# Kernel tuning notes

Measured on AMD Instinct MI355X. Metric: run time of the kernel, lower is better.

## Reference

```python
import jax, jax.numpy as jnp
import numpy as np

COST_CLASS = 1.0
COST_BBOX = 5.0
COST_GIOU = 2.0


def box_cxcywh_to_xyxy(b):
    cx, cy, w, h = b[..., 0], b[..., 1], b[..., 2], b[..., 3]
    return jnp.stack([cx - 0.5 * w, cy - 0.5 * h, cx + 0.5 * w, cy + 0.5 * h], axis=-1)


def generalized_box_iou(a, b):
    # a: [N,4] xyxy, b: [M,4] xyxy -> [N,M]
    area_a = (a[:, 2] - a[:, 0]) * (a[:, 3] - a[:, 1])
    area_b = (b[:, 2] - b[:, 0]) * (b[:, 3] - b[:, 1])
    lt = jnp.maximum(a[:, None, :2], b[None, :, :2])
    rb = jnp.minimum(a[:, None, 2:], b[None, :, 2:])
    wh = jnp.clip(rb - lt, 0.0)
    inter = wh[..., 0] * wh[..., 1]
    union = area_a[:, None] + area_b[None, :] - inter
    iou = inter / union
    lt_e = jnp.minimum(a[:, None, :2], b[None, :, :2])
    rb_e = jnp.maximum(a[:, None, 2:], b[None, :, 2:])
    wh_e = jnp.clip(rb_e - lt_e, 0.0)
    area_e = wh_e[..., 0] * wh_e[..., 1]
    return iou - (area_e - union) / area_e


def setup_inputs() -> dict:
    key = jax.random.key(0)
    k1, k2, k3, k4 = jax.random.split(key, 4)
    bs, Q, C, T = 64, 300, 13, 32
    pred_logits = jax.random.normal(k1, (bs, Q, C), dtype=jnp.float32)
    pred_boxes = jax.random.uniform(k2, (bs, Q, 4), dtype=jnp.float32)
    tgt_boxes = jax.random.uniform(k3, (bs, T, 4), dtype=jnp.float32)
    tgt_ids = jax.random.randint(k4, (bs, T), 0, 12, dtype=jnp.int64)
    return {"pred_logits": pred_logits, "pred_boxes": pred_boxes,
            "tgt_boxes": tgt_boxes, "tgt_ids": tgt_ids}


def reference(pred_logits, pred_boxes, tgt_boxes, tgt_ids):
    bs, Q, _ = pred_logits.shape
    T = tgt_boxes.shape[1]
    out_prob = jax.nn.softmax(pred_logits.reshape(bs * Q, -1), axis=-1)
    out_bbox = pred_boxes.reshape(bs * Q, 4)
    tgt_bbox = tgt_boxes.reshape(bs * T, 4)
    tgt_id = tgt_ids.reshape(bs * T)
    # classification cost: -P[tgt class]  [bs*Q, bs*T]
    cost_class = -out_prob[:, tgt_id]
    # L1 cdist  [bs*Q, bs*T]
    cost_bbox = jnp.sum(jnp.abs(out_bbox[:, None, :] - tgt_bbox[None, :, :]), axis=-1)
    # -GIoU  [bs*Q, bs*T]
    cost_giou = -generalized_box_iou(box_cxcywh_to_xyxy(out_bbox),
                                     box_cxcywh_to_xyxy(tgt_bbox))
    C = COST_CLASS * cost_class + COST_BBOX * cost_bbox + COST_GIOU * cost_giou
    C = C.reshape(bs, Q, bs * T)
    # faithful to the source: each batch element keeps the FIRST size[i] columns
    # (uniform sizes => [:, :, :T])
    return C[:, :, :T]
```

## Files before the change

kernel.cpp:

```cpp
#include <hip/hip_runtime.h>


constexpr int QN = 300;
constexpr int NC = 13;
constexpr int T  = 32;
constexpr float W_BBOX = 5.0f;
constexpr float W_GIOU = 2.0f;

constexpr int BLK = 256;
constexpr int TPQ = 8;
constexpr int TGT = T / TPQ;

__global__ __launch_bounds__(BLK) void matcher_kernel(
    const float* __restrict__ pred_logits,
    const float* __restrict__ pred_boxes,
    const float* __restrict__ tgt_boxes,
    const int*   __restrict__ tgt_ids,
    float* __restrict__ out)
{
    const int gtid = blockIdx.x * BLK + threadIdx.x;
    const int q   = gtid >> 3;
    const int sub = gtid & 7;

    const float* lg = pred_logits + (size_t)q * NC;
    float l[NC];
    #pragma unroll
    for (int c = 0; c < NC; ++c) l[c] = lg[c];
    float m = l[0];
    #pragma unroll
    for (int c = 1; c < NC; ++c) m = fmaxf(m, l[c]);
    float s = 0.0f;
    #pragma unroll
    for (int c = 0; c < NC; ++c) { l[c] = __expf(l[c] - m); s += l[c]; }
    float inv = 1.0f / s;
    #pragma unroll
    for (int c = 0; c < NC; ++c) l[c] *= inv;

    float4 pb = *(const float4*)(pred_boxes + (size_t)q * 4);
    float px0 = pb.x - 0.5f * pb.z, py0 = pb.y - 0.5f * pb.w;
    float px1 = pb.x + 0.5f * pb.z, py1 = pb.y + 0.5f * pb.w;
    float parea = (px1 - px0) * (py1 - py0);

    const int t0 = sub * TGT;
    float res[TGT];
    #pragma unroll
    for (int k = 0; k < TGT; ++k) {
        const int t = t0 + k;
        float4 tb = *(const float4*)(tgt_boxes + t * 4);
        int id = tgt_ids[t];

        float p = l[0];
        #pragma unroll
        for (int c = 1; c < NC; ++c) p = (id == c) ? l[c] : p;

        float cb = fabsf(pb.x - tb.x) + fabsf(pb.y - tb.y)
                 + fabsf(pb.z - tb.z) + fabsf(pb.w - tb.w);

        float tx0 = tb.x - 0.5f * tb.z, ty0 = tb.y - 0.5f * tb.w;
        float tx1 = tb.x + 0.5f * tb.z, ty1 = tb.y + 0.5f * tb.w;
        float tarea = (tx1 - tx0) * (ty1 - ty0);

        float ltx = fmaxf(px0, tx0), lty = fmaxf(py0, ty0);
        float rbx = fminf(px1, tx1), rby = fminf(py1, ty1);
        float iw = fmaxf(rbx - ltx, 0.0f), ih = fmaxf(rby - lty, 0.0f);
        float inter = iw * ih;
        float uni = parea + tarea - inter;
        float iou = inter / uni;
        float ex0 = fminf(px0, tx0), ey0 = fminf(py0, ty0);
        float ex1 = fmaxf(px1, tx1), ey1 = fmaxf(py1, ty1);
        float earea = (ex1 - ex0) * (ey1 - ey0);
        float giou = iou - (earea - uni) / earea;

        res[k] = -p + W_BBOX * cb - W_GIOU * giou;
    }

    float* o = out + (size_t)q * T + t0;
    float4 v; v.x = res[0]; v.y = res[1]; v.z = res[2]; v.w = res[3];
    *(float4*)o = v;
}

extern "C" void kernel_launch(void* const* d_in, const int* in_sizes, int n_in,
                              void* d_out, int out_size, void* d_ws, size_t ws_size,
                              hipStream_t stream) {
    const float* pred_logits = (const float*)d_in[0];
    const float* pred_boxes  = (const float*)d_in[1];
    const float* tgt_boxes   = (const float*)d_in[2];
    const int*   tgt_ids     = (const int*)d_in[3];
    float* out = (float*)d_out;

    const int total = 64 * QN * TPQ;
    const int grid = total / BLK;
    matcher_kernel<<<grid, BLK, 0, stream>>>(pred_logits, pred_boxes,
                                             tgt_boxes, tgt_ids, out);
}
```

Before: 9.910 us.

## Split softmax across 16 lanes per query with shuffles and lane gather

Each query is now handled by 16 lanes instead of 8. Each lane loads one logit, and the max and sum reductions run cooperatively through xor shuffles, replacing the redundant per-thread 13-element softmax. The class probability for each target is fetched by a lane shuffle indexed by the target id rather than a 13-way select chain. Each lane now computes 2 targets instead of 4, which doubles the thread count and adds shuffle latency, and the stores become float2 instead of float4.

```diff
diff --git a/kernel.cpp b/kernel.cpp
--- a/kernel.cpp
+++ b/kernel.cpp
@@ -8,8 +8,30 @@
 constexpr float W_GIOU = 2.0f;
 
 constexpr int BLK = 256;
-constexpr int TPQ = 8;
-constexpr int TGT = T / TPQ;
+constexpr int LPQ = 16;
+constexpr int QPB = BLK / LPQ;
+
+__device__ __forceinline__ float cost_one(
+    float4 pb, float px0, float py0, float px1, float py1, float parea,
+    float4 tb, float p)
+{
+    float cb = fabsf(pb.x - tb.x) + fabsf(pb.y - tb.y)
+             + fabsf(pb.z - tb.z) + fabsf(pb.w - tb.w);
+    float tx0 = tb.x - 0.5f * tb.z, ty0 = tb.y - 0.5f * tb.w;
+    float tx1 = tb.x + 0.5f * tb.z, ty1 = tb.y + 0.5f * tb.w;
+    float tarea = (tx1 - tx0) * (ty1 - ty0);
+    float ltx = fmaxf(px0, tx0), lty = fmaxf(py0, ty0);
+    float rbx = fminf(px1, tx1), rby = fminf(py1, ty1);
+    float iw = fmaxf(rbx - ltx, 0.0f), ih = fmaxf(rby - lty, 0.0f);
+    float inter = iw * ih;
+    float uni = parea + tarea - inter;
+    float iou = inter / uni;
+    float ex0 = fminf(px0, tx0), ey0 = fminf(py0, ty0);
+    float ex1 = fmaxf(px1, tx1), ey1 = fmaxf(py1, ty1);
+    float earea = (ex1 - ex0) * (ey1 - ey0);
+    float giou = iou - (earea - uni) / earea;
+    return -p + W_BBOX * cb - W_GIOU * giou;
+}
 
 __global__ __launch_bounds__(BLK) void matcher_kernel(
     const float* __restrict__ pred_logits,
@@ -18,65 +40,38 @@
     const int*   __restrict__ tgt_ids,
     float* __restrict__ out)
 {
-    const int gtid = blockIdx.x * BLK + threadIdx.x;
-    const int q   = gtid >> 3;
-    const int sub = gtid & 7;
+    const int tid = threadIdx.x;
+    const int j = tid & (LPQ - 1);
+    const int q = blockIdx.x * QPB + (tid >> 4);
 
-    const float* lg = pred_logits + (size_t)q * NC;
-    float l[NC];
+    float lv = (j < NC) ? pred_logits[(size_t)q * NC + j] : -1e30f;
+    float m = lv;
     #pragma unroll
-    for (int c = 0; c < NC; ++c) l[c] = lg[c];
-    float m = l[0];
+    for (int mask = 8; mask >= 1; mask >>= 1)
+        m = fmaxf(m, __shfl_xor(m, mask, LPQ));
+    float e = (j < NC) ? __expf(lv - m) : 0.0f;
+    float s = e;
     #pragma unroll
-    for (int c = 1; c < NC; ++c) m = fmaxf(m, l[c]);
-    float s = 0.0f;
-    #pragma unroll
-    for (int c = 0; c < NC; ++c) { l[c] = __expf(l[c] - m); s += l[c]; }
-    float inv = 1.0f / s;
-    #pragma unroll
-    for (int c = 0; c < NC; ++c) l[c] *= inv;
+    for (int mask = 8; mask >= 1; mask >>= 1)
+        s += __shfl_xor(s, mask, LPQ);
+    float prob = e / s;
 
     float4 pb = *(const float4*)(pred_boxes + (size_t)q * 4);
     float px0 = pb.x - 0.5f * pb.z, py0 = pb.y - 0.5f * pb.w;
     float px1 = pb.x + 0.5f * pb.z, py1 = pb.y + 0.5f * pb.w;
     float parea = (px1 - px0) * (py1 - py0);
 
-    const int t0 = sub * TGT;
-    float res[TGT];
-    #pragma unroll
-    for (int k = 0; k < TGT; ++k) {
-        const int t = t0 + k;
-        float4 tb = *(const float4*)(tgt_boxes + t * 4);
-        int id = tgt_ids[t];
+    int2 ids = *(const int2*)(tgt_ids + 2 * j);
+    float4 tb0 = *(const float4*)(tgt_boxes + (size_t)(2 * j) * 4);
+    float4 tb1 = *(const float4*)(tgt_boxes + (size_t)(2 * j + 1) * 4);
+    float p0 = __shfl(prob, ids.x, LPQ);
+    float p1 = __shfl(prob, ids.y, LPQ);
 
-        float p = l[0];
-        #pragma unroll
-        for (int c = 1; c < NC; ++c) p = (id == c) ? l[c] : p;
+    float c0 = cost_one(pb, px0, py0, px1, py1, parea, tb0, p0);
+    float c1 = cost_one(pb, px0, py0, px1, py1, parea, tb1, p1);
 
-        float cb = fabsf(pb.x - tb.x) + fabsf(pb.y - tb.y)
-                 + fabsf(pb.z - tb.z) + fabsf(pb.w - tb.w);
-
-        float tx0 = tb.x - 0.5f * tb.z, ty0 = tb.y - 0.5f * tb.w;
-        float tx1 = tb.x + 0.5f * tb.z, ty1 = tb.y + 0.5f * tb.w;
-        float tarea = (tx1 - tx0) * (ty1 - ty0);
-
-        float ltx = fmaxf(px0, tx0), lty = fmaxf(py0, ty0);
-        float rbx = fminf(px1, tx1), rby = fminf(py1, ty1);
-        float iw = fmaxf(rbx - ltx, 0.0f), ih = fmaxf(rby - lty, 0.0f);
-        float inter = iw * ih;
-        float uni = parea + tarea - inter;
-        float iou = inter / uni;
-        float ex0 = fminf(px0, tx0), ey0 = fminf(py0, ty0);
-        float ex1 = fmaxf(px1, tx1), ey1 = fmaxf(py1, ty1);
-        float earea = (ex1 - ex0) * (ey1 - ey0);
-        float giou = iou - (earea - uni) / earea;
-
-        res[k] = -p + W_BBOX * cb - W_GIOU * giou;
-    }
-
-    float* o = out + (size_t)q * T + t0;
-    float4 v; v.x = res[0]; v.y = res[1]; v.z = res[2]; v.w = res[3];
-    *(float4*)o = v;
+    float2 v; v.x = c0; v.y = c1;
+    *(float2*)(out + (size_t)q * T + 2 * j) = v;
 }
 
 extern "C" void kernel_launch(void* const* d_in, const int* in_sizes, int n_in,
@@ -88,8 +83,8 @@
     const int*   tgt_ids     = (const int*)d_in[3];
     float* out = (float*)d_out;
 
-    const int total = 64 * QN * TPQ;
-    const int grid = total / BLK;
+    const int total_q = 64 * QN;
+    const int grid = total_q / QPB;
     matcher_kernel<<<grid, BLK, 0, stream>>>(pred_logits, pred_boxes,
                                              tgt_boxes, tgt_ids, out);
 }
```

Result: no change. 9.824 us (-0.9%).
